# Performance work log

Hardware: AMD Instinct MI355X
Metric: run time of the kernel (lower is better)

The kernel has to match this reference:

```python
import jax, jax.numpy as jnp
import numpy as np

B, S, E = 2, 2049, 512
H, WIN = 8, 1024
D = E // H


def setup_inputs() -> dict:
    key = jax.random.key(0)
    ks = jax.random.split(key, 11)
    sc = 0.02
    return {
        "x": jax.random.normal(ks[0], (B, S, E), dtype=jnp.float32),
        "Wq": jax.random.normal(ks[1], (E, E), dtype=jnp.float32) * sc,
        "bq": jnp.zeros((E,), dtype=jnp.float32),
        "Wk": jax.random.normal(ks[2], (E, E), dtype=jnp.float32) * sc,
        "bk": jnp.zeros((E,), dtype=jnp.float32),
        "Wv": jax.random.normal(ks[3], (E, E), dtype=jnp.float32) * sc,
        "bv": jnp.zeros((E,), dtype=jnp.float32),
        "Wo": jax.random.normal(ks[4], (E, E), dtype=jnp.float32) * sc,
        "bo": jnp.zeros((E,), dtype=jnp.float32),
        "w_gate": jax.random.normal(ks[5], (2 * E,), dtype=jnp.float32) * sc,
        "b_gate": jnp.zeros((), dtype=jnp.float32),
    }


def reference(x, Wq, bq, Wk, bk, Wv, bv, Wo, bo, w_gate, b_gate):
    scale = D ** -0.5
    q_flat = x @ Wq + bq  # [B,S,E]
    k_flat = x @ Wk + bk
    v_flat = x @ Wv + bv
    q = q_flat.reshape(B, S, H, D).transpose(0, 2, 1, 3)  # [B,H,S,D]
    k = k_flat.reshape(B, S, H, D).transpose(0, 2, 1, 3)
    v = v_flat.reshape(B, S, H, D).transpose(0, 2, 1, 3)

    scores = jnp.einsum("bhqd,bhkd->bhqk", q, k) * scale  # [B,H,S,S]

    # Gaussian positional bias: -0.5*|i-j|^2/sigma^2, sigma = window/2
    pos = jnp.arange(S)
    dist = jnp.abs(pos[:, None] - pos[None, :]).astype(jnp.float32)
    sigma = WIN / 2.0
    bias = -0.5 * dist ** 2 / (sigma ** 2)  # [S,S]
    scores = scores + bias[None, None]

    # Pairwise gate: sigmoid(concat(q_i,k_j) @ w + b) == sigmoid(q_i.wq + k_j.wk + b)
    gq = q_flat @ w_gate[:E]       # [B,S]
    gk = k_flat @ w_gate[E:]       # [B,S]
    gates = jax.nn.sigmoid(gq[:, :, None] + gk[:, None, :] + b_gate)  # [B,S,S]
    scores = scores * gates[:, None]  # broadcast over heads

    local_mask = jnp.where(dist <= WIN, 0.0, -jnp.inf).astype(jnp.float32)
    scores = scores + local_mask[None, None]

    attn = jax.nn.softmax(scores, axis=-1)
    out = jnp.einsum("bhqk,bhkd->bhqd", attn, v)  # [B,H,S,D]
    out = out.transpose(0, 2, 1, 3).reshape(B, S, E)
    return out @ Wo + bo
```

## Files before the change

kernel.cpp:

```cpp
#include <hip/hip_runtime.h>
#include <cstdint>
#include <cstddef>

#define B_ 2
#define S_ 2049
#define E_ 512
#define H_ 8
#define WIN_ 1024
#define MROWS (B_*S_)
#define SP_ 2176
#define GBUFN 4104
#define HS_ (H_*S_)
#define BHS_ (B_*H_*S_)

typedef unsigned short ushort_t;
typedef __attribute__((ext_vector_type(8))) short bf16x8;
typedef __attribute__((ext_vector_type(4))) float f32x4;

#define MFMA16(a,b,c) __builtin_amdgcn_mfma_f32_16x16x32_bf16(a,b,c,0,0,0)

__device__ __forceinline__ ushort_t f2bf(float f) {
  unsigned int u = __float_as_uint(f);
  u += 0x7fffu + ((u >> 16) & 1u);
  return (ushort_t)(u >> 16);
}
__device__ __forceinline__ float bf2f(ushort_t h) {
  return __uint_as_float(((unsigned int)h) << 16);
}

__global__ __launch_bounds__(256) void convert_w_kernel(
    const float* __restrict__ W0, const float* __restrict__ W1,
    const float* __restrict__ W2, const float* __restrict__ W3,
    ushort_t* __restrict__ Wt_all, ushort_t* __restrict__ WoHi)
{
  __shared__ float tile[32][33];
  int z = blockIdx.z;
  const float* W = (z == 0) ? W0 : (z == 1) ? W1 : (z == 2) ? W2 : W3;
  int k0 = blockIdx.x * 32, n0 = blockIdx.y * 32;
  int r = threadIdx.x >> 5, c = threadIdx.x & 31;
#pragma unroll
  for (int i = 0; i < 4; ++i) {
    int rr = r + i * 8;
    tile[rr][c] = W[(size_t)(k0 + rr) * E_ + n0 + c];
  }
  __syncthreads();
#pragma unroll
  for (int i = 0; i < 4; ++i) {
    int rr = r + i * 8;
    float v = tile[c][rr];
    size_t dst = (size_t)(n0 + rr) * E_ + k0 + c;
    if (z < 3) Wt_all[(size_t)z * E_ * E_ + dst] = f2bf(v);
    else       WoHi[dst] = f2bf(v);
  }
}

__global__ __launch_bounds__(256) void gemm_qkv_kernel(
    const float* __restrict__ x, const ushort_t* __restrict__ Wt_all,
    const float* __restrict__ bq, const float* __restrict__ bk,
    const float* __restrict__ bv, const float* __restrict__ wg,
    ushort_t* __restrict__ qkb, ushort_t* __restrict__ vT,
    float* __restrict__ gq_acc, float* __restrict__ gk_acc)
{
  __shared__ __align__(16) ushort_t As[64][40];
  __shared__ __align__(16) ushort_t Bs[128][40];
  int tid = threadIdx.x;
  int lane = tid & 63, w = tid >> 6;
  int l15 = lane & 15, quad = lane >> 4;
  int wm = (w & 1) * 32, wn = (w >> 1) * 64;
  int z = blockIdx.z;
  const ushort_t* Wt = Wt_all + (size_t)z * E_ * E_;
  const float* bias = (z == 0) ? bq : (z == 1) ? bk : bv;
  int bm = blockIdx.x * 64, bn = blockIdx.y * 128;

  int ar = tid >> 2, acq = (tid & 3) * 8;
  int am = bm + ar; if (am >= MROWS) am = MROWS - 1;
  const float* ap = x + (size_t)am * E_ + acq;
  int br = tid >> 1, bcq = (tid & 1) * 16;
  const ushort_t* bp = Wt + (size_t)(bn + br) * E_ + bcq;

  const f32x4 fz = {0.f, 0.f, 0.f, 0.f};
  f32x4 acc[2][4];
#pragma unroll
  for (int mt = 0; mt < 2; ++mt)
#pragma unroll
    for (int nt = 0; nt < 4; ++nt) acc[mt][nt] = fz;

  float4 pa0 = *(const float4*)ap, pa1 = *(const float4*)(ap + 4);
  int4  pb0 = *(const int4*)bp,   pb1 = *(const int4*)(bp + 8);

  for (int k0 = 0; k0 < E_; k0 += 32) {
    __syncthreads();
    int kn = (k0 + 32 < E_) ? (k0 + 32) : k0;
    float4 na0 = *(const float4*)(ap + kn), na1 = *(const float4*)(ap + kn + 4);
    int4  nb0 = *(const int4*)(bp + kn),   nb1 = *(const int4*)(bp + kn + 8);
    union { int4 v; ushort_t u[8]; } cv;
    cv.u[0] = f2bf(pa0.x); cv.u[1] = f2bf(pa0.y); cv.u[2] = f2bf(pa0.z); cv.u[3] = f2bf(pa0.w);
    cv.u[4] = f2bf(pa1.x); cv.u[5] = f2bf(pa1.y); cv.u[6] = f2bf(pa1.z); cv.u[7] = f2bf(pa1.w);
    *(int4*)&As[ar][acq] = cv.v;
    *(int4*)&Bs[br][bcq] = pb0; *(int4*)&Bs[br][bcq + 8] = pb1;
    __syncthreads();
    bf16x8 a[2], bfr[4];
#pragma unroll
    for (int mt = 0; mt < 2; ++mt) a[mt] = *(const bf16x8*)&As[wm + mt * 16 + l15][quad * 8];
#pragma unroll
    for (int nt = 0; nt < 4; ++nt) bfr[nt] = *(const bf16x8*)&Bs[wn + nt * 16 + l15][quad * 8];
#pragma unroll
    for (int mt = 0; mt < 2; ++mt)
#pragma unroll
      for (int nt = 0; nt < 4; ++nt)
        acc[mt][nt] = MFMA16(a[mt], bfr[nt], acc[mt][nt]);
    pa0 = na0; pa1 = na1; pb0 = nb0; pb1 = nb1;
  }

  float bb[4];
#pragma unroll
  for (int nt = 0; nt < 4; ++nt) bb[nt] = bias[bn + wn + nt * 16 + l15];

  if (z < 2) {
    ushort_t* C = qkb + (size_t)z * MROWS * E_;
#pragma unroll
    for (int mt = 0; mt < 2; ++mt)
#pragma unroll
      for (int nt = 0; nt < 4; ++nt)
#pragma unroll
        for (int r = 0; r < 4; ++r) {
          int m = bm + wm + mt * 16 + quad * 4 + r;
          if (m < MROWS)
            C[(size_t)m * E_ + bn + wn + nt * 16 + l15] = f2bf(acc[mt][nt][r] + bb[nt]);
        }
    const float* wgp = wg + (size_t)z * E_;
    float wv[4];
#pragma unroll
    for (int nt = 0; nt < 4; ++nt) wv[nt] = wgp[bn + wn + nt * 16 + l15];
    float* gacc = (z == 0) ? gq_acc : gk_acc;
#pragma unroll
    for (int mt = 0; mt < 2; ++mt)
#pragma unroll
      for (int r = 0; r < 4; ++r) {
        float s = 0.f;
#pragma unroll
        for (int nt = 0; nt < 4; ++nt) s = fmaf(acc[mt][nt][r] + bb[nt], wv[nt], s);
        s += __shfl_xor(s, 1, 16); s += __shfl_xor(s, 2, 16);
        s += __shfl_xor(s, 4, 16); s += __shfl_xor(s, 8, 16);
        int m = bm + wm + mt * 16 + quad * 4 + r;
        if (l15 == 0 && m < MROWS) atomicAdd(&gacc[m], s);
      }
  } else {
#pragma unroll
    for (int mt = 0; mt < 2; ++mt)
#pragma unroll
      for (int nt = 0; nt < 4; ++nt) {
        int dg = bn + wn + nt * 16 + l15;
        int h = dg >> 6, d = dg & 63;
#pragma unroll
        for (int r = 0; r < 4; ++r) {
          int m = bm + wm + mt * 16 + quad * 4 + r;
          if (m < MROWS) {
            int b = (m >= S_) ? 1 : 0;
            int i = m - b * S_;
            vT[((size_t)(b * H_ + h) * 64 + d) * SP_ + i] = f2bf(acc[mt][nt][r] + bb[nt]);
          }
        }
      }
  }
}

__global__ __launch_bounds__(256) void attn_kernel(
    const ushort_t* __restrict__ qb, const ushort_t* __restrict__ kb,
    const ushort_t* __restrict__ vT, const float* __restrict__ gq_raw,
    const float* __restrict__ gk_raw, const float* __restrict__ bgate,
    float* __restrict__ Opart, float* __restrict__ Lpart)
{
  __shared__ __align__(16) ushort_t Ks[64][72];
  __shared__ __align__(16) ushort_t Vt[64][72];
  __shared__ __align__(16) ushort_t Ps[4][16][72];
  __shared__ float gbs[1088];

  int tid = threadIdx.x;
  int lane = tid & 63, w = tid >> 6;
  int l15 = lane & 15, quad = lane >> 4;

  int sub = blockIdx.x & 31;
  int qidx = blockIdx.x >> 5;
  int off = (qidx + 1) >> 1;
  int qt = 16 + ((qidx & 1) ? -off : off);
  int bh = sub & 15, half = sub >> 4;
  int h = bh & 7, b = bh >> 3;
  int i0 = qt * 64;
  const float coef = -0.5f / (512.f * 512.f);

  int i = i0 + w * 16 + l15;
  int ic = (i < S_) ? i : S_ - 1;
  bf16x8 qf0 = *(const bf16x8*)&qb[((size_t)(b * S_ + ic)) * E_ + h * 64 + quad * 8];
  bf16x8 qf1 = *(const bf16x8*)&qb[((size_t)(b * S_ + ic)) * E_ + h * 64 + 32 + quad * 8];
#pragma unroll
  for (int e = 0; e < 8; ++e) {
    qf0[e] = (short)f2bf(bf2f((ushort_t)qf0[e]) * 0.125f);
    qf1[e] = (short)f2bf(bf2f((ushort_t)qf1[e]) * 0.125f);
  }
  float av = __expf(-(gq_raw[b * S_ + ic] + bgate[0]));
  float fdi = (i < S_) ? (float)i : -1e5f;

  int jlo = i0 - WIN_; if (jlo < 0) jlo = 0;
  int jt_lo = jlo >> 6;
  int jhi = i0 + 63 + WIN_; if (jhi > S_ - 1) jhi = S_ - 1;
  int jt_hi = jhi >> 6;
  int L = jt_hi - jt_lo + 1;
  int Lh = (L + 1) >> 1;
  int myLo = half ? (jt_lo + Lh) : jt_lo;
  int myHi = half ? jt_hi : (jt_lo + Lh - 1);
  int jbase = myLo << 6;
  int nwin = (myHi - myLo + 1) << 6;

  for (int tt = tid; tt < nwin; tt += 256) {
    int j = jbase + tt; int jc = (j < S_) ? j : S_ - 1;
    gbs[tt] = __expf(-gk_raw[b * S_ + jc]);
  }

  int srow = tid >> 2, scol = (tid & 3) * 16;
  const ushort_t* kb_base = kb + (size_t)b * S_ * E_ + h * 64 + scol;
  const ushort_t* vb_base = vT + ((size_t)(b * H_ + h) * 64 + srow) * SP_ + scol;

  int4 ka0, ka1, va0, va1;
  {
    int jc0 = jbase + srow; if (jc0 > S_ - 1) jc0 = S_ - 1;
    const int4* kp = (const int4*)(kb_base + (size_t)jc0 * E_);
    ka0 = kp[0]; ka1 = kp[1];
    const int4* vp = (const int4*)(vb_base + jbase);
    va0 = vp[0]; va1 = vp[1];
  }

  const f32x4 fz = {0.f, 0.f, 0.f, 0.f};
  f32x4 Ov[4] = {fz, fz, fz, fz};
  float l_run = 0.f;

  for (int jt = myLo; jt <= myHi; ++jt) {
    int j0 = jt << 6;
    __syncthreads();
    int jn = (jt < myHi) ? ((jt + 1) << 6) : j0;
    int jcn = jn + srow; if (jcn > S_ - 1) jcn = S_ - 1;
    const int4* kp = (const int4*)(kb_base + (size_t)jcn * E_);
    int4 nk0 = kp[0], nk1 = kp[1];
    const int4* vp = (const int4*)(vb_base + jn);
    int4 nv0 = vp[0], nv1 = vp[1];
    *(int4*)&Ks[srow][scol] = ka0; *(int4*)&Ks[srow][scol + 8] = ka1;
    *(int4*)&Vt[srow][scol] = va0; *(int4*)&Vt[srow][scol + 8] = va1;
    __syncthreads();

    f32x4 st[4];
#pragma unroll
    for (int nt = 0; nt < 4; ++nt) {
      bf16x8 kf0 = *(const bf16x8*)&Ks[nt * 16 + l15][quad * 8];
      bf16x8 kf1 = *(const bf16x8*)&Ks[nt * 16 + l15][32 + quad * 8];
      f32x4 s = MFMA16(kf0, qf0, fz);
      st[nt] = MFMA16(kf1, qf1, s);
    }

    bool full = ((j0 + 63 - i0) <= WIN_) && ((i0 + 63 - j0) <= WIN_)
                && (j0 + 63 < S_) && (i0 + 63 < S_);
    float ps = 0.f;
    float jq = (float)(j0 + quad * 4);
    if (full) {
#pragma unroll
      for (int nt = 0; nt < 4; ++nt) {
        f32x4 g4 = *(const f32x4*)&gbs[(j0 - jbase) + nt * 16 + quad * 4];
#pragma unroll
        for (int r = 0; r < 4; ++r) {
          float f = fdi - (jq + (float)(nt * 16 + r));
          float gate = __builtin_amdgcn_rcpf(fmaf(av, g4[r], 1.f));
          float p = __expf(fmaf(f * f, coef, st[nt][r]) * gate);
          st[nt][r] = p; ps += p;
        }
      }
    } else {
#pragma unroll
      for (int nt = 0; nt < 4; ++nt) {
        f32x4 g4 = *(const f32x4*)&gbs[(j0 - jbase) + nt * 16 + quad * 4];
#pragma unroll
        for (int r = 0; r < 4; ++r) {
          int j = j0 + nt * 16 + quad * 4 + r;
          float fj = (j < S_) ? (float)j : 1e5f;
          float f = fdi - fj;
          float gate = __builtin_amdgcn_rcpf(fmaf(av, g4[r], 1.f));
          float t = fmaf(f * f, coef, st[nt][r]) * gate;
          t = (__builtin_fabsf(f) <= 1024.f) ? t : -1e30f;
          float p = __expf(t);
          st[nt][r] = p; ps += p;
        }
      }
    }
    ps += __shfl_xor(ps, 16);
    ps += __shfl_xor(ps, 32);
    l_run += ps;

#pragma unroll
    for (int nt = 0; nt < 4; ++nt) {
      uint2 pk;
      pk.x = (unsigned int)f2bf(st[nt][0]) | ((unsigned int)f2bf(st[nt][1]) << 16);
      pk.y = (unsigned int)f2bf(st[nt][2]) | ((unsigned int)f2bf(st[nt][3]) << 16);
      *(uint2*)&Ps[w][l15][nt * 16 + quad * 4] = pk;
    }
    bf16x8 p0 = *(const bf16x8*)&Ps[w][l15][quad * 8];
    bf16x8 p1 = *(const bf16x8*)&Ps[w][l15][32 + quad * 8];
#pragma unroll
    for (int nt = 0; nt < 4; ++nt) {
      bf16x8 v0 = *(const bf16x8*)&Vt[nt * 16 + l15][quad * 8];
      bf16x8 v1 = *(const bf16x8*)&Vt[nt * 16 + l15][32 + quad * 8];
      Ov[nt] = MFMA16(p0, v0, Ov[nt]);
      Ov[nt] = MFMA16(p1, v1, Ov[nt]);
    }
    ka0 = nk0; ka1 = nk1; va0 = nv0; va1 = nv1;
  }

  if (lane < 16) {
    int irow = i0 + w * 16 + lane;
    if (irow < S_)
      Lpart[(size_t)half * BHS_ + (size_t)(b * H_ + h) * S_ + irow] = l_run;
  }
#pragma unroll
  for (int r = 0; r < 4; ++r) {
    int irow = i0 + w * 16 + quad * 4 + r;
    if (irow < S_) {
      size_t base = ((size_t)half * BHS_ + (size_t)(b * H_ + h) * S_ + irow) * (size_t)64;
#pragma unroll
      for (int nt = 0; nt < 4; ++nt)
        Opart[base + nt * 16 + l15] = Ov[nt][r];
    }
  }
}

__global__ __launch_bounds__(256) void combine_kernel(
    const float* __restrict__ Opart, const float* __restrict__ Lpart,
    ushort_t* __restrict__ ahi, ushort_t* __restrict__ alo)
{
  int tid = threadIdx.x;
  int gi = blockIdx.x * 16 + (tid >> 4);
  int d4 = tid & 15;
  int b = gi / HS_;
  int rem = gi - b * HS_;
  int h = rem / S_;
  int i = rem - h * S_;
  size_t p0 = (size_t)(b * H_ + h) * S_ + i;
  size_t p1 = p0 + (size_t)BHS_;
  float inv = __builtin_amdgcn_rcpf(Lpart[p0] + Lpart[p1]);
  float4 o1 = *(const float4*)&Opart[p0 * 64 + d4 * 4];
  float4 o2 = *(const float4*)&Opart[p1 * 64 + d4 * 4];
  float o[4] = {(o1.x + o2.x) * inv, (o1.y + o2.y) * inv,
                (o1.z + o2.z) * inv, (o1.w + o2.w) * inv};
  ushort4 hi, lo;
  hi.x = f2bf(o[0]); lo.x = f2bf(o[0] - bf2f(hi.x));
  hi.y = f2bf(o[1]); lo.y = f2bf(o[1] - bf2f(hi.y));
  hi.z = f2bf(o[2]); lo.z = f2bf(o[2] - bf2f(hi.z));
  hi.w = f2bf(o[3]); lo.w = f2bf(o[3] - bf2f(hi.w));
  size_t oidx = ((size_t)b * S_ + i) * E_ + h * 64 + d4 * 4;
  *(ushort4*)&ahi[oidx] = hi;
  *(ushort4*)&alo[oidx] = lo;
}

__global__ __launch_bounds__(256) void gemm_out_kernel(
    const ushort_t* __restrict__ Ahi, const ushort_t* __restrict__ Alo,
    const ushort_t* __restrict__ Whi, const float* __restrict__ bias,
    float* __restrict__ C)
{
  __shared__ __align__(16) ushort_t AsH[64][40];
  __shared__ __align__(16) ushort_t AsL[64][40];
  __shared__ __align__(16) ushort_t BsW[64][40];
  int tid = threadIdx.x;
  int lane = tid & 63, w = tid >> 6;
  int l15 = lane & 15, quad = lane >> 4;
  int bm = blockIdx.x * 64, bn = blockIdx.y * 64;
  int sr = tid >> 2, sc = (tid & 3) * 8;
  int am = bm + sr; if (am >= MROWS) am = MROWS - 1;
  const ushort_t* ahp = Ahi + (size_t)am * E_ + sc;
  const ushort_t* alp = Alo + (size_t)am * E_ + sc;
  const ushort_t* bp  = Whi + (size_t)(bn + sr) * E_ + sc;

  const f32x4 fz = {0.f, 0.f, 0.f, 0.f};
  f32x4 acc[4] = {fz, fz, fz, fz};

  int4 ph = *(const int4*)ahp, pl = *(const int4*)alp, pb = *(const int4*)bp;

  for (int k0 = 0; k0 < E_; k0 += 32) {
    __syncthreads();
    int kn = (k0 + 32 < E_) ? (k0 + 32) : k0;
    int4 nh = *(const int4*)(ahp + kn);
    int4 nl = *(const int4*)(alp + kn);
    int4 nb = *(const int4*)(bp + kn);
    *(int4*)&AsH[sr][sc] = ph;
    *(int4*)&AsL[sr][sc] = pl;
    *(int4*)&BsW[sr][sc] = pb;
    __syncthreads();
    bf16x8 ah = *(const bf16x8*)&AsH[w * 16 + l15][quad * 8];
    bf16x8 al = *(const bf16x8*)&AsL[w * 16 + l15][quad * 8];
#pragma unroll
    for (int nt = 0; nt < 4; ++nt) {
      bf16x8 bw = *(const bf16x8*)&BsW[nt * 16 + l15][quad * 8];
      acc[nt] = MFMA16(ah, bw, acc[nt]);
      acc[nt] = MFMA16(al, bw, acc[nt]);
    }
    ph = nh; pl = nl; pb = nb;
  }
#pragma unroll
  for (int nt = 0; nt < 4; ++nt) {
    float bb = bias[bn + nt * 16 + l15];
#pragma unroll
    for (int r = 0; r < 4; ++r) {
      int m = bm + w * 16 + quad * 4 + r;
      if (m < MROWS)
        C[(size_t)m * E_ + bn + nt * 16 + l15] = acc[nt][r] + bb;
    }
  }
}

extern "C" void kernel_launch(void* const* d_in, const int* in_sizes, int n_in,
                              void* d_out, int out_size, void* d_ws, size_t ws_size,
                              hipStream_t stream) {
  const float* x  = (const float*)d_in[0];
  const float* Wq = (const float*)d_in[1];
  const float* bq = (const float*)d_in[2];
  const float* Wk = (const float*)d_in[3];
  const float* bk = (const float*)d_in[4];
  const float* Wv = (const float*)d_in[5];
  const float* bv = (const float*)d_in[6];
  const float* Wo = (const float*)d_in[7];
  const float* bo = (const float*)d_in[8];
  const float* wg = (const float*)d_in[9];
  const float* bg = (const float*)d_in[10];

  char* p = (char*)d_ws;
  ushort_t* Wt_all = (ushort_t*)p; p += (size_t)3 * E_ * E_ * 2;
  ushort_t* WoHi   = (ushort_t*)p; p += (size_t)E_ * E_ * 2;
  ushort_t* qkb    = (ushort_t*)p; p += (size_t)2 * MROWS * E_ * 2;
  ushort_t* vT     = (ushort_t*)p; p += (size_t)B_ * H_ * 64 * SP_ * 2;
  float*    gq_acc = (float*)p;    p += (size_t)GBUFN * 4;
  float*    gk_acc = (float*)p;    p += (size_t)GBUFN * 4;
  float*    Opart  = (float*)p;    p += (size_t)2 * BHS_ * 64 * 4;
  float*    Lpart  = (float*)p;    p += (size_t)2 * BHS_ * 4;
  ushort_t* aHi    = (ushort_t*)p; p += (size_t)MROWS * E_ * 2;
  ushort_t* aLo    = (ushort_t*)p; p += (size_t)MROWS * E_ * 2;

  hipMemsetAsync(gq_acc, 0, 2 * (size_t)GBUFN * 4, stream);
  hipLaunchKernelGGL(convert_w_kernel, dim3(16, 16, 4), dim3(256), 0, stream,
                     Wq, Wk, Wv, Wo, Wt_all, WoHi);
  hipLaunchKernelGGL(gemm_qkv_kernel, dim3(65, 4, 3), dim3(256), 0, stream,
                     x, Wt_all, bq, bk, bv, wg, qkb, vT, gq_acc, gk_acc);
  hipLaunchKernelGGL(attn_kernel, dim3(33 * 32), dim3(256), 0, stream,
                     qkb, qkb + (size_t)MROWS * E_, vT, gq_acc, gk_acc, bg,
                     Opart, Lpart);
  hipLaunchKernelGGL(combine_kernel, dim3(2049), dim3(256), 0, stream,
                     Opart, Lpart, aHi, aLo);
  hipLaunchKernelGGL(gemm_out_kernel, dim3(65, 8), dim3(256), 0, stream,
                     aHi, aLo, WoHi, bo, (float*)d_out);
}
```

Baseline: 175.6 us.

## Split attention keys three ways, fuse combine into output GEMM, coalesce V transpose

Attention key ranges are now split across three blocks per query tile instead of two, so more blocks are in flight. The separate combine kernel is removed: the output GEMM reads the three partial outputs and row sums, normalises them and splits them into hi/lo bf16 while loading its A tile. The QKV GEMM tiles rows per batch and writes the V transpose through LDS with vector stores, and the memset is folded into the weight-conversion kernel. These changes cut launches and the aHi/aLo round trip, at the cost of more partial-output traffic and a fused GEMM that no longer prefetches its A operand.

```diff
diff --git a/kernel.cpp b/kernel.cpp
--- a/kernel.cpp
+++ b/kernel.cpp
@@ -10,7 +10,6 @@
 #define MROWS (B_*S_)
 #define SP_ 2176
 #define GBUFN 4104
-#define HS_ (H_*S_)
 #define BHS_ (B_*H_*S_)
 
 typedef unsigned short ushort_t;
@@ -31,10 +30,15 @@
 __global__ __launch_bounds__(256) void convert_w_kernel(
     const float* __restrict__ W0, const float* __restrict__ W1,
     const float* __restrict__ W2, const float* __restrict__ W3,
-    ushort_t* __restrict__ Wt_all, ushort_t* __restrict__ WoHi)
+    ushort_t* __restrict__ Wt_all, ushort_t* __restrict__ WoHi,
+    float* __restrict__ gacc)
 {
   __shared__ float tile[32][33];
   int z = blockIdx.z;
+  if (z == 3) {
+    int gz = (blockIdx.x * 16 + blockIdx.y) * 256 + threadIdx.x;
+    if (gz < 2 * GBUFN) gacc[gz] = 0.f;
+  }
   const float* W = (z == 0) ? W0 : (z == 1) ? W1 : (z == 2) ? W2 : W3;
   int k0 = blockIdx.x * 32, n0 = blockIdx.y * 32;
   int r = threadIdx.x >> 5, c = threadIdx.x & 31;
@@ -59,7 +63,7 @@
     const float* __restrict__ bq, const float* __restrict__ bk,
     const float* __restrict__ bv, const float* __restrict__ wg,
     ushort_t* __restrict__ qkb, ushort_t* __restrict__ vT,
-    float* __restrict__ gq_acc, float* __restrict__ gk_acc)
+    float* __restrict__ gacc)
 {
   __shared__ __align__(16) ushort_t As[64][40];
   __shared__ __align__(16) ushort_t Bs[128][40];
@@ -70,11 +74,15 @@
   int z = blockIdx.z;
   const ushort_t* Wt = Wt_all + (size_t)z * E_ * E_;
   const float* bias = (z == 0) ? bq : (z == 1) ? bk : bv;
-  int bm = blockIdx.x * 64, bn = blockIdx.y * 128;
+  int bt = blockIdx.x;
+  int bg2 = bt / 33;
+  int bm = (bt - bg2 * 33) * 64;
+  int bn = blockIdx.y * 128;
+  size_t rowbase = (size_t)bg2 * S_;
 
   int ar = tid >> 2, acq = (tid & 3) * 8;
-  int am = bm + ar; if (am >= MROWS) am = MROWS - 1;
-  const float* ap = x + (size_t)am * E_ + acq;
+  int ai = bm + ar; if (ai >= S_) ai = S_ - 1;
+  const float* ap = x + (rowbase + ai) * E_ + acq;
   int br = tid >> 1, bcq = (tid & 1) * 16;
   const ushort_t* bp = Wt + (size_t)(bn + br) * E_ + bcq;
 
@@ -124,15 +132,15 @@
       for (int nt = 0; nt < 4; ++nt)
 #pragma unroll
         for (int r = 0; r < 4; ++r) {
-          int m = bm + wm + mt * 16 + quad * 4 + r;
-          if (m < MROWS)
-            C[(size_t)m * E_ + bn + wn + nt * 16 + l15] = f2bf(acc[mt][nt][r] + bb[nt]);
+          int i = bm + wm + mt * 16 + quad * 4 + r;
+          if (i < S_)
+            C[(rowbase + i) * E_ + bn + wn + nt * 16 + l15] = f2bf(acc[mt][nt][r] + bb[nt]);
         }
     const float* wgp = wg + (size_t)z * E_;
     float wv[4];
 #pragma unroll
     for (int nt = 0; nt < 4; ++nt) wv[nt] = wgp[bn + wn + nt * 16 + l15];
-    float* gacc = (z == 0) ? gq_acc : gk_acc;
+    float* gp = gacc + (size_t)z * GBUFN;
 #pragma unroll
     for (int mt = 0; mt < 2; ++mt)
 #pragma unroll
@@ -142,26 +150,46 @@
         for (int nt = 0; nt < 4; ++nt) s = fmaf(acc[mt][nt][r] + bb[nt], wv[nt], s);
         s += __shfl_xor(s, 1, 16); s += __shfl_xor(s, 2, 16);
         s += __shfl_xor(s, 4, 16); s += __shfl_xor(s, 8, 16);
-        int m = bm + wm + mt * 16 + quad * 4 + r;
-        if (l15 == 0 && m < MROWS) atomicAdd(&gacc[m], s);
+        int i = bm + wm + mt * 16 + quad * 4 + r;
+        if (l15 == 0 && i < S_) atomicAdd(&gp[rowbase + i], s);
       }
   } else {
-#pragma unroll
-    for (int mt = 0; mt < 2; ++mt)
-#pragma unroll
-      for (int nt = 0; nt < 4; ++nt) {
-        int dg = bn + wn + nt * 16 + l15;
-        int h = dg >> 6, d = dg & 63;
-#pragma unroll
-        for (int r = 0; r < 4; ++r) {
-          int m = bm + wm + mt * 16 + quad * 4 + r;
-          if (m < MROWS) {
-            int b = (m >= S_) ? 1 : 0;
-            int i = m - b * S_;
-            vT[((size_t)(b * H_ + h) * 64 + d) * SP_ + i] = f2bf(acc[mt][nt][r] + bb[nt]);
+    ushort_t* lt = &Bs[0][0];
+    int ti = tid >> 2, tc = (tid & 3) * 16;
+#pragma unroll
+    for (int hh = 0; hh < 2; ++hh) {
+      __syncthreads();
+      if ((w >> 1) == hh) {
+#pragma unroll
+        for (int mt = 0; mt < 2; ++mt)
+#pragma unroll
+          for (int nt = 0; nt < 4; ++nt) {
+            int d = nt * 16 + l15;
+#pragma unroll
+            for (int r = 0; r < 4; ++r) {
+              int il = wm + mt * 16 + quad * 4 + r;
+              lt[d * 72 + il] = f2bf(acc[mt][nt][r] + bb[nt]);
+            }
           }
+      }
+      __syncthreads();
+      int hg = (bn >> 6) + hh;
+      union { int4 q[2]; ushort_t u[16]; } tv;
+      tv.q[0] = *(const int4*)&lt[ti * 72 + tc];
+      tv.q[1] = *(const int4*)&lt[ti * 72 + tc + 8];
+      size_t vrow = ((size_t)(bg2 * H_ + hg) * 64 + ti) * SP_;
+#pragma unroll
+      for (int c8 = 0; c8 < 2; ++c8) {
+        int i2 = bm + tc + c8 * 8;
+        if (i2 + 7 < S_) {
+          *(int4*)&vT[vrow + i2] = tv.q[c8];
+        } else {
+#pragma unroll
+          for (int e = 0; e < 8; ++e)
+            if (i2 + e < S_) vT[vrow + i2 + e] = tv.u[c8 * 8 + e];
         }
       }
+    }
   }
 }
 
@@ -174,17 +202,17 @@
   __shared__ __align__(16) ushort_t Ks[64][72];
   __shared__ __align__(16) ushort_t Vt[64][72];
   __shared__ __align__(16) ushort_t Ps[4][16][72];
-  __shared__ float gbs[1088];
+  __shared__ float gbs[704];
 
   int tid = threadIdx.x;
   int lane = tid & 63, w = tid >> 6;
   int l15 = lane & 15, quad = lane >> 4;
 
-  int sub = blockIdx.x & 31;
-  int qidx = blockIdx.x >> 5;
+  int sub = blockIdx.x % 48;
+  int qidx = blockIdx.x / 48;
   int off = (qidx + 1) >> 1;
   int qt = 16 + ((qidx & 1) ? -off : off);
-  int bh = sub & 15, half = sub >> 4;
+  int bh = sub & 15, third = sub >> 4;
   int h = bh & 7, b = bh >> 3;
   int i0 = qt * 64;
   const float coef = -0.5f / (512.f * 512.f);
@@ -206,11 +234,12 @@
   int jhi = i0 + 63 + WIN_; if (jhi > S_ - 1) jhi = S_ - 1;
   int jt_hi = jhi >> 6;
   int L = jt_hi - jt_lo + 1;
-  int Lh = (L + 1) >> 1;
-  int myLo = half ? (jt_lo + Lh) : jt_lo;
-  int myHi = half ? jt_hi : (jt_lo + Lh - 1);
+  int n0 = (L + 2) / 3, n1 = (L + 1) / 3;
+  int myLo = jt_lo + ((third == 0) ? 0 : (third == 1) ? n0 : n0 + n1);
+  int cnt = (third == 0) ? n0 : (third == 1) ? n1 : L - n0 - n1;
+  int myHi = myLo + cnt - 1;
   int jbase = myLo << 6;
-  int nwin = (myHi - myLo + 1) << 6;
+  int nwin = cnt << 6;
 
   for (int tt = tid; tt < nwin; tt += 256) {
     int j = jbase + tt; int jc = (j < S_) ? j : S_ - 1;
@@ -315,13 +344,13 @@
   if (lane < 16) {
     int irow = i0 + w * 16 + lane;
     if (irow < S_)
-      Lpart[(size_t)half * BHS_ + (size_t)(b * H_ + h) * S_ + irow] = l_run;
+      Lpart[(size_t)third * BHS_ + (size_t)(b * H_ + h) * S_ + irow] = l_run;
   }
 #pragma unroll
   for (int r = 0; r < 4; ++r) {
     int irow = i0 + w * 16 + quad * 4 + r;
     if (irow < S_) {
-      size_t base = ((size_t)half * BHS_ + (size_t)(b * H_ + h) * S_ + irow) * (size_t)64;
+      size_t base = ((size_t)third * BHS_ + (size_t)(b * H_ + h) * S_ + irow) * 64;
 #pragma unroll
       for (int nt = 0; nt < 4; ++nt)
         Opart[base + nt * 16 + l15] = Ov[nt][r];
@@ -329,66 +358,67 @@
   }
 }
 
-__global__ __launch_bounds__(256) void combine_kernel(
+__global__ __launch_bounds__(256) void gemm_out_kernel(
     const float* __restrict__ Opart, const float* __restrict__ Lpart,
-    ushort_t* __restrict__ ahi, ushort_t* __restrict__ alo)
-{
-  int tid = threadIdx.x;
-  int gi = blockIdx.x * 16 + (tid >> 4);
-  int d4 = tid & 15;
-  int b = gi / HS_;
-  int rem = gi - b * HS_;
-  int h = rem / S_;
-  int i = rem - h * S_;
-  size_t p0 = (size_t)(b * H_ + h) * S_ + i;
-  size_t p1 = p0 + (size_t)BHS_;
-  float inv = __builtin_amdgcn_rcpf(Lpart[p0] + Lpart[p1]);
-  float4 o1 = *(const float4*)&Opart[p0 * 64 + d4 * 4];
-  float4 o2 = *(const float4*)&Opart[p1 * 64 + d4 * 4];
-  float o[4] = {(o1.x + o2.x) * inv, (o1.y + o2.y) * inv,
-                (o1.z + o2.z) * inv, (o1.w + o2.w) * inv};
-  ushort4 hi, lo;
-  hi.x = f2bf(o[0]); lo.x = f2bf(o[0] - bf2f(hi.x));
-  hi.y = f2bf(o[1]); lo.y = f2bf(o[1] - bf2f(hi.y));
-  hi.z = f2bf(o[2]); lo.z = f2bf(o[2] - bf2f(hi.z));
-  hi.w = f2bf(o[3]); lo.w = f2bf(o[3] - bf2f(hi.w));
-  size_t oidx = ((size_t)b * S_ + i) * E_ + h * 64 + d4 * 4;
-  *(ushort4*)&ahi[oidx] = hi;
-  *(ushort4*)&alo[oidx] = lo;
-}
-
-__global__ __launch_bounds__(256) void gemm_out_kernel(
-    const ushort_t* __restrict__ Ahi, const ushort_t* __restrict__ Alo,
     const ushort_t* __restrict__ Whi, const float* __restrict__ bias,
     float* __restrict__ C)
 {
   __shared__ __align__(16) ushort_t AsH[64][40];
   __shared__ __align__(16) ushort_t AsL[64][40];
   __shared__ __align__(16) ushort_t BsW[64][40];
+  __shared__ float invL[64][8];
   int tid = threadIdx.x;
   int lane = tid & 63, w = tid >> 6;
   int l15 = lane & 15, quad = lane >> 4;
   int bm = blockIdx.x * 64, bn = blockIdx.y * 64;
-  int sr = tid >> 2, sc = (tid & 3) * 8;
-  int am = bm + sr; if (am >= MROWS) am = MROWS - 1;
-  const ushort_t* ahp = Ahi + (size_t)am * E_ + sc;
-  const ushort_t* alp = Alo + (size_t)am * E_ + sc;
-  const ushort_t* bp  = Whi + (size_t)(bn + sr) * E_ + sc;
+
+  for (int idx = tid; idx < 512; idx += 256) {
+    int r = idx >> 3, hh = idx & 7;
+    int m = bm + r; if (m >= MROWS) m = MROWS - 1;
+    int b2 = (m >= S_) ? 1 : 0;
+    int i = m - b2 * S_;
+    size_t li = (size_t)(b2 * H_ + hh) * S_ + i;
+    float l = Lpart[li] + Lpart[(size_t)BHS_ + li] + Lpart[2 * (size_t)BHS_ + li];
+    invL[r][hh] = 1.f / l;
+  }
+
+  int sr = tid >> 2, scq = (tid & 3) * 8;
+  int m = bm + sr; if (m >= MROWS) m = MROWS - 1;
+  int b2 = (m >= S_) ? 1 : 0;
+  int i = m - b2 * S_;
+  size_t obase = (((size_t)(b2 * H_) * S_) + i) * 64;
+  const ushort_t* bp = Whi + (size_t)(bn + sr) * E_ + scq;
 
   const f32x4 fz = {0.f, 0.f, 0.f, 0.f};
   f32x4 acc[4] = {fz, fz, fz, fz};
-
-  int4 ph = *(const int4*)ahp, pl = *(const int4*)alp, pb = *(const int4*)bp;
+  const size_t TOFF = (size_t)BHS_ * 64;
 
   for (int k0 = 0; k0 < E_; k0 += 32) {
     __syncthreads();
-    int kn = (k0 + 32 < E_) ? (k0 + 32) : k0;
-    int4 nh = *(const int4*)(ahp + kn);
-    int4 nl = *(const int4*)(alp + kn);
-    int4 nb = *(const int4*)(bp + kn);
-    *(int4*)&AsH[sr][sc] = ph;
-    *(int4*)&AsL[sr][sc] = pl;
-    *(int4*)&BsW[sr][sc] = pb;
+    int e0 = k0 + scq;
+    int h = e0 >> 6, d = e0 & 63;
+    const float* op = Opart + obase + (size_t)h * (S_ * 64) + d;
+    float4 a0 = *(const float4*)op;
+    float4 a1 = *(const float4*)(op + 4);
+    float4 q0 = *(const float4*)(op + TOFF);
+    float4 q1 = *(const float4*)(op + TOFF + 4);
+    float4 c0 = *(const float4*)(op + 2 * TOFF);
+    float4 c1 = *(const float4*)(op + 2 * TOFF + 4);
+    float sc = invL[sr][h];
+    float o[8] = {(a0.x + q0.x + c0.x) * sc, (a0.y + q0.y + c0.y) * sc,
+                  (a0.z + q0.z + c0.z) * sc, (a0.w + q0.w + c0.w) * sc,
+                  (a1.x + q1.x + c1.x) * sc, (a1.y + q1.y + c1.y) * sc,
+                  (a1.z + q1.z + c1.z) * sc, (a1.w + q1.w + c1.w) * sc};
+    union { int4 v; ushort_t u[8]; } hi, lo;
+#pragma unroll
+    for (int e = 0; e < 8; ++e) {
+      ushort_t hv = f2bf(o[e]);
+      hi.u[e] = hv;
+      lo.u[e] = f2bf(o[e] - bf2f(hv));
+    }
+    *(int4*)&AsH[sr][scq] = hi.v;
+    *(int4*)&AsL[sr][scq] = lo.v;
+    *(int4*)&BsW[sr][scq] = *(const int4*)(bp + k0);
     __syncthreads();
     bf16x8 ah = *(const bf16x8*)&AsH[w * 16 + l15][quad * 8];
     bf16x8 al = *(const bf16x8*)&AsL[w * 16 + l15][quad * 8];
@@ -398,16 +428,15 @@
       acc[nt] = MFMA16(ah, bw, acc[nt]);
       acc[nt] = MFMA16(al, bw, acc[nt]);
     }
-    ph = nh; pl = nl; pb = nb;
   }
 #pragma unroll
   for (int nt = 0; nt < 4; ++nt) {
     float bb = bias[bn + nt * 16 + l15];
 #pragma unroll
     for (int r = 0; r < 4; ++r) {
-      int m = bm + w * 16 + quad * 4 + r;
-      if (m < MROWS)
-        C[(size_t)m * E_ + bn + nt * 16 + l15] = acc[nt][r] + bb;
+      int mm = bm + w * 16 + quad * 4 + r;
+      if (mm < MROWS)
+        C[(size_t)mm * E_ + bn + nt * 16 + l15] = acc[nt][r] + bb;
     }
   }
 }
@@ -432,23 +461,17 @@
   ushort_t* WoHi   = (ushort_t*)p; p += (size_t)E_ * E_ * 2;
   ushort_t* qkb    = (ushort_t*)p; p += (size_t)2 * MROWS * E_ * 2;
   ushort_t* vT     = (ushort_t*)p; p += (size_t)B_ * H_ * 64 * SP_ * 2;
-  float*    gq_acc = (float*)p;    p += (size_t)GBUFN * 4;
-  float*    gk_acc = (float*)p;    p += (size_t)GBUFN * 4;
-  float*    Opart  = (float*)p;    p += (size_t)2 * BHS_ * 64 * 4;
-  float*    Lpart  = (float*)p;    p += (size_t)2 * BHS_ * 4;
-  ushort_t* aHi    = (ushort_t*)p; p += (size_t)MROWS * E_ * 2;
-  ushort_t* aLo    = (ushort_t*)p; p += (size_t)MROWS * E_ * 2;
-
-  hipMemsetAsync(gq_acc, 0, 2 * (size_t)GBUFN * 4, stream);
+  float*    gacc   = (float*)p;    p += (size_t)2 * GBUFN * 4;
+  float*    Opart  = (float*)p;    p += (size_t)3 * BHS_ * 64 * 4;
+  float*    Lpart  = (float*)p;    p += (size_t)3 * BHS_ * 4;
+
   hipLaunchKernelGGL(convert_w_kernel, dim3(16, 16, 4), dim3(256), 0, stream,
-                     Wq, Wk, Wv, Wo, Wt_all, WoHi);
-  hipLaunchKernelGGL(gemm_qkv_kernel, dim3(65, 4, 3), dim3(256), 0, stream,
-                     x, Wt_all, bq, bk, bv, wg, qkb, vT, gq_acc, gk_acc);
-  hipLaunchKernelGGL(attn_kernel, dim3(33 * 32), dim3(256), 0, stream,
-                     qkb, qkb + (size_t)MROWS * E_, vT, gq_acc, gk_acc, bg,
+                     Wq, Wk, Wv, Wo, Wt_all, WoHi, gacc);
+  hipLaunchKernelGGL(gemm_qkv_kernel, dim3(66, 4, 3), dim3(256), 0, stream,
+                     x, Wt_all, bq, bk, bv, wg, qkb, vT, gacc);
+  hipLaunchKernelGGL(attn_kernel, dim3(33 * 48), dim3(256), 0, stream,
+                     qkb, qkb + (size_t)MROWS * E_, vT, gacc, gacc + GBUFN, bg,
                      Opart, Lpart);
-  hipLaunchKernelGGL(combine_kernel, dim3(2049), dim3(256), 0, stream,
-                     Opart, Lpart, aHi, aLo);
   hipLaunchKernelGGL(gemm_out_kernel, dim3(65, 8), dim3(256), 0, stream,
-                     aHi, aLo, WoHi, bo, (float*)d_out);
-}
+                     Opart, Lpart, WoHi, bo, (float*)d_out);
+}
```

Result: slower. 193.0 us (+9.9%).
